# Performance work log

Measured on AMD Instinct MI355X. Metric: run time of the kernel, lower is better.

The kernel has to match this reference:

```python
import jax, jax.numpy as jnp
import numpy as np
import math

DIM = 1536
HEAD_DIM = 128
N_HEADS = DIM // HEAD_DIM
B, S = 2, 2048
F, H, W = 8, 16, 16  # F*H*W == S
MAX_POS = 1024
EPS = 1e-6


def _make_freqs():
    # complex rotary freqs per Wan convention, split [22,21,21] over head_dim/2=64
    c = HEAD_DIM // 2
    sizes = [c - 2 * (c // 3), c // 3, c // 3]
    theta = 10000.0
    parts = []
    for s in sizes:
        inv = 1.0 / theta ** (np.arange(s, dtype=np.float64) / s)
        ang = np.arange(MAX_POS, dtype=np.float64)[:, None] * inv[None, :]
        parts.append(np.stack([np.cos(ang), np.sin(ang)], axis=-1))
    return jnp.asarray(np.concatenate(parts, axis=1), dtype=jnp.float32)  # [MAX_POS, 64, 2]


def setup_inputs() -> dict:
    key = jax.random.key(0)
    ks = jax.random.split(key, 12)
    std = 1.0 / math.sqrt(DIM)
    inp = {
        "x": jax.random.normal(ks[0], (B, S, DIM), jnp.float32),
        "seq_lens": jnp.full((B,), S, jnp.int32),
        "grid_sizes": jnp.tile(jnp.array([[F, H, W]], jnp.int32), (B, 1)),
        "freqs": _make_freqs(),
        "Wq": jax.random.normal(ks[1], (DIM, DIM), jnp.float32) * std,
        "bq": jnp.zeros((DIM,), jnp.float32),
        "Wk": jax.random.normal(ks[2], (DIM, DIM), jnp.float32) * std,
        "bk": jnp.zeros((DIM,), jnp.float32),
        "Wv": jax.random.normal(ks[3], (DIM, DIM), jnp.float32) * std,
        "bv": jnp.zeros((DIM,), jnp.float32),
        "Wo": jax.random.normal(ks[4], (DIM, DIM), jnp.float32) * std,
        "bo": jnp.zeros((DIM,), jnp.float32),
        "wq_norm": jnp.ones((DIM,), jnp.float32),
        "wk_norm": jnp.ones((DIM,), jnp.float32),
    }
    return inp


def _rmsnorm(x, w):
    x32 = x.astype(jnp.float32)
    return x32 * jax.lax.rsqrt(jnp.mean(x32 * x32, axis=-1, keepdims=True) + EPS) * w


def _rope_apply(x, grid_sizes, freqs):
    # x: [B, S, N, D]; grid sizes uniform across batch -> vectorized (no per-sample loop)
    f, h, w = (int(v) for v in np.asarray(grid_sizes)[0])
    s_rot = f * h * w
    Bx, Sx, N, D = x.shape
    c = D // 2
    s0, s1 = c - 2 * (c // 3), c // 3
    cos, sin = freqs[..., 0], freqs[..., 1]

    def grid_cs(t):  # build [s_rot, c] table
        tf = jnp.broadcast_to(t[:f, None, None, :s0], (f, h, w, s0))
        th = jnp.broadcast_to(t[None, :h, None, s0:s0 + s1], (f, h, w, s1))
        tw = jnp.broadcast_to(t[None, None, :w, s0 + s1:s0 + 2 * s1], (f, h, w, s1))
        return jnp.concatenate([tf, th, tw], axis=-1).reshape(s_rot, 1, c)

    fc, fs = grid_cs(cos), grid_cs(sin)  # [s_rot, 1, c]
    xr = x[:, :s_rot].astype(jnp.float32).reshape(Bx, s_rot, N, c, 2)
    a, b = xr[..., 0], xr[..., 1]
    out = jnp.stack([a * fc - b * fs, a * fs + b * fc], axis=-1).reshape(Bx, s_rot, N, D)
    if s_rot < Sx:
        out = jnp.concatenate([out, x[:, s_rot:].astype(jnp.float32)], axis=1)
    return out


def reference(x, seq_lens, grid_sizes, freqs, Wq, bq, Wk, bk, Wv, bv, Wo, bo, wq_norm, wk_norm):
    Bx, Sx, dim = x.shape
    N, D = N_HEADS, HEAD_DIM
    q = _rmsnorm(x @ Wq.T + bq, wq_norm).reshape(Bx, Sx, N, D)
    k = _rmsnorm(x @ Wk.T + bk, wk_norm).reshape(Bx, Sx, N, D)
    v = (x @ Wv.T + bv).reshape(Bx, Sx, N, D)
    q = _rope_apply(q, grid_sizes, freqs)
    k = _rope_apply(k, grid_sizes, freqs)
    scores = jnp.einsum("bsnd,btnd->bnst", q, k) / math.sqrt(D)  # [B,N,S,S]
    kmask = jnp.arange(Sx)[None, :] < seq_lens[:, None]          # [B,S] over keys
    scores = jnp.where(kmask[:, None, None, :], scores, -1e30)
    attn = jax.nn.softmax(scores, axis=-1)
    out = jnp.einsum("bnst,btnd->bsnd", attn, v).reshape(Bx, Sx, dim)
    return out @ Wo.T + bo
```

## Files before the change

kernel.cpp:

```cpp
#include <hip/hip_runtime.h>

typedef __attribute__((ext_vector_type(8))) short bf16x8;
typedef __attribute__((ext_vector_type(8))) unsigned short ushort8;
typedef __attribute__((ext_vector_type(4))) float f32x4;
typedef __attribute__((ext_vector_type(16))) float f32x16;
typedef unsigned short u16;
typedef unsigned int u32;

__device__ inline float bf2f(u16 u) {
    unsigned int x = ((unsigned int)u) << 16;
    float f; __builtin_memcpy(&f, &x, 4); return f;
}
__device__ inline u16 f2bf(float f) {
    unsigned int x; __builtin_memcpy(&x, &f, 4);
    unsigned int r = (x + 0x7FFFu + ((x >> 16) & 1u)) >> 16;
    return (u16)r;
}
__device__ inline u32 cvtpk(float lo, float hi) {
    u32 r;
    asm("v_cvt_pk_bf16_f32 %0, %1, %2" : "=v"(r) : "v"(lo), "v"(hi));
    return r;
}
__device__ inline void store_out(u16* p, float v) { *p = f2bf(v); }
__device__ inline void store_out(float* p, float v) { *p = v; }

__global__ __launch_bounds__(256) void prep_kernel(const float* __restrict__ x,
                                                   const float* __restrict__ Wq, const float* __restrict__ Wk,
                                                   const float* __restrict__ Wv, const float* __restrict__ Wo,
                                                   const float* __restrict__ bq, const float* __restrict__ bk,
                                                   const float* __restrict__ bv, const float* __restrict__ freqs,
                                                   u16* __restrict__ xb,
                                                   u16* __restrict__ wqkv, u16* __restrict__ wob,
                                                   float* __restrict__ bqkv, float* __restrict__ rope) {
    int bid = blockIdx.x, t = threadIdx.x;
    if (bid < 7680) {
        const float* src;
        u16* dst;
        size_t j;
        if (bid < 3072) {
            src = x; dst = xb; j = (size_t)bid * 256 + t;
        } else {
            size_t i = (size_t)(bid - 3072) * 256 + t;
            int seg = (int)(i / 294912); j = i - (size_t)seg * 294912;
            src = (seg == 0) ? Wq : (seg == 1) ? Wk : (seg == 2) ? Wv : Wo;
            dst = (seg < 3) ? (wqkv + (size_t)seg * 2359296) : wob;
        }
        float4 a = *(const float4*)(src + j * 8);
        float4 b = *(const float4*)(src + j * 8 + 4);
        ushort8 o;
        o[0] = f2bf(a.x); o[1] = f2bf(a.y); o[2] = f2bf(a.z); o[3] = f2bf(a.w);
        o[4] = f2bf(b.x); o[5] = f2bf(b.y); o[6] = f2bf(b.z); o[7] = f2bf(b.w);
        *(ushort8*)(dst + j * 8) = o;
    } else if (bid < 8192) {
        int i = (bid - 7680) * 256 + t;
        int s = i >> 6, j = i & 63;
        int fi = s >> 8, hi = (s >> 4) & 15, wi = s & 15;
        int pos = (j < 22) ? fi : ((j < 43) ? hi : wi);
        rope[s * 128 + j * 2]     = freqs[pos * 128 + j * 2];
        rope[s * 128 + j * 2 + 1] = freqs[pos * 128 + j * 2 + 1];
    } else {
#pragma unroll
        for (int it = 0; it < 18; ++it) {
            int j = it * 256 + t;
            bqkv[j] = (j < 1536) ? bq[j] : ((j < 3072) ? bk[j - 1536] : bv[j - 3072]);
        }
    }
}

template <typename OutT>
__global__ __launch_bounds__(256) void gemm_db(const u16* __restrict__ A, const u16* __restrict__ Bw,
                                               const float* __restrict__ bias, OutT* __restrict__ C,
                                               int M, int N, int K) {
    __shared__ __align__(16) u16 As[2][4096];
    __shared__ __align__(16) u16 Bs[2][4096];
    const int tid = threadIdx.x;
    const int w = tid >> 6, l = tid & 63;
    const int lg = l >> 4, li = l & 15;
    const int row0 = blockIdx.x * 128, col0 = blockIdx.y * 128;
    const int wr = (w >> 1) * 64, wc = (w & 1) * 64;
    const int nt = K >> 5;

    f32x4 acc[4][4] = {};

    auto STAGE = [&](int bi, int t) {
        int k0 = t << 5;
#pragma unroll
        for (int c = 0; c < 2; ++c) {
            int idx = c * 256 + tid;
            int r = idx >> 2;
            int clog = (idx & 3) ^ ((r >> 1) & 3);
            __builtin_amdgcn_global_load_lds(
                (const __attribute__((address_space(1))) void*)(A + (size_t)(row0 + r) * K + k0 + clog * 8),
                (__attribute__((address_space(3))) void*)((char*)&As[0][0] + bi * 8192 + c * 4096 + w * 1024), 16, 0, 0);
            __builtin_amdgcn_global_load_lds(
                (const __attribute__((address_space(1))) void*)(Bw + (size_t)(col0 + r) * K + k0 + clog * 8),
                (__attribute__((address_space(3))) void*)((char*)&Bs[0][0] + bi * 8192 + c * 4096 + w * 1024), 16, 0, 0);
        }
    };

    const int rchunk = (lg ^ ((li >> 1) & 3)) * 8;
    STAGE(0, 0);
    for (int tb = 0; tb < nt; tb += 2) {
#pragma unroll
        for (int j = 0; j < 2; ++j) {
            const int t = tb + j;
            if (t + 1 < nt) {
                STAGE((j + 1) & 1, t + 1);
                asm volatile("s_waitcnt vmcnt(4)" ::: "memory");
            } else {
                asm volatile("s_waitcnt vmcnt(0)" ::: "memory");
            }
            __builtin_amdgcn_s_barrier();
            __builtin_amdgcn_sched_barrier(0);
            const u16* as = &As[j][0];
            const u16* bs = &Bs[j][0];
            bf16x8 af[4], bfr[4];
#pragma unroll
            for (int m = 0; m < 4; ++m) af[m] = *(const bf16x8*)(as + (wr + m * 16 + li) * 32 + rchunk);
#pragma unroll
            for (int n = 0; n < 4; ++n) bfr[n] = *(const bf16x8*)(bs + (wc + n * 16 + li) * 32 + rchunk);
#pragma unroll
            for (int m = 0; m < 4; ++m)
#pragma unroll
                for (int n = 0; n < 4; ++n)
                    acc[m][n] = __builtin_amdgcn_mfma_f32_16x16x32_bf16(af[m], bfr[n], acc[m][n], 0, 0, 0);
            __builtin_amdgcn_sched_barrier(0);
            __builtin_amdgcn_s_barrier();
        }
    }

#pragma unroll
    for (int m = 0; m < 4; ++m) {
#pragma unroll
        for (int n = 0; n < 4; ++n) {
#pragma unroll
            for (int j = 0; j < 4; ++j) {
                int r = row0 + wr + m * 16 + lg * 4 + j;
                int cc = col0 + wc + n * 16 + li;
                float v = acc[m][n][j] + bias[cc];
                store_out(&C[(size_t)r * N + cc], v);
            }
        }
    }
}

template <typename OutT>
__global__ __launch_bounds__(256) void gemm_bt(const u16* __restrict__ A, const u16* __restrict__ Bw,
                                               const float* __restrict__ bias, OutT* __restrict__ C,
                                               int M, int N, int K) {
    __shared__ __align__(16) u16 As[3][4096];
    __shared__ __align__(16) u16 Bs[3][4096];
    const int tid = threadIdx.x;
    const int w = tid >> 6, l = tid & 63;
    const int lg = l >> 4, li = l & 15;
    const int row0 = blockIdx.x * 128, col0 = blockIdx.y * 128;
    const int wr = (w >> 1) * 64, wc = (w & 1) * 64;
    const int nt = K >> 5;

    f32x4 acc[4][4] = {};

    auto STAGE = [&](int bi, int t) {
        int k0 = t << 5;
#pragma unroll
        for (int c = 0; c < 2; ++c) {
            int idx = c * 256 + tid;
            int r = idx >> 2;
            int clog = (idx & 3) ^ ((r >> 1) & 3);
            __builtin_amdgcn_global_load_lds(
                (const __attribute__((address_space(1))) void*)(A + (size_t)(row0 + r) * K + k0 + clog * 8),
                (__attribute__((address_space(3))) void*)((char*)&As[0][0] + bi * 8192 + c * 4096 + w * 1024), 16, 0, 0);
            __builtin_amdgcn_global_load_lds(
                (const __attribute__((address_space(1))) void*)(Bw + (size_t)(col0 + r) * K + k0 + clog * 8),
                (__attribute__((address_space(3))) void*)((char*)&Bs[0][0] + bi * 8192 + c * 4096 + w * 1024), 16, 0, 0);
        }
    };

    const int rchunk = (lg ^ ((li >> 1) & 3)) * 8;
    STAGE(0, 0);
    STAGE(1, 1);
    for (int tb = 0; tb < nt; tb += 3) {
#pragma unroll
        for (int j = 0; j < 3; ++j) {
            const int t = tb + j;
            if (t + 2 < nt) {
                STAGE((j + 2) % 3, t + 2);
                asm volatile("s_waitcnt vmcnt(8)" ::: "memory");
            } else if (t + 1 < nt) {
                asm volatile("s_waitcnt vmcnt(4)" ::: "memory");
            } else {
                asm volatile("s_waitcnt vmcnt(0)" ::: "memory");
            }
            __builtin_amdgcn_s_barrier();
            __builtin_amdgcn_sched_barrier(0);
            const u16* as = &As[j][0];
            const u16* bs = &Bs[j][0];
            bf16x8 af[4], bfr[4];
#pragma unroll
            for (int m = 0; m < 4; ++m) af[m] = *(const bf16x8*)(as + (wr + m * 16 + li) * 32 + rchunk);
#pragma unroll
            for (int n = 0; n < 4; ++n) bfr[n] = *(const bf16x8*)(bs + (wc + n * 16 + li) * 32 + rchunk);
#pragma unroll
            for (int m = 0; m < 4; ++m)
#pragma unroll
                for (int n = 0; n < 4; ++n)
                    acc[m][n] = __builtin_amdgcn_mfma_f32_16x16x32_bf16(af[m], bfr[n], acc[m][n], 0, 0, 0);
            __builtin_amdgcn_sched_barrier(0);
            __builtin_amdgcn_s_barrier();
        }
    }

#pragma unroll
    for (int m = 0; m < 4; ++m) {
#pragma unroll
        for (int n = 0; n < 4; ++n) {
#pragma unroll
            for (int j = 0; j < 4; ++j) {
                int r = row0 + wr + m * 16 + lg * 4 + j;
                int cc = col0 + wc + n * 16 + li;
                float v = acc[m][n][j] + bias[cc];
                store_out(&C[(size_t)r * N + cc], v);
            }
        }
    }
}

__global__ __launch_bounds__(256) void rmsview_kernel(const u16* __restrict__ qkv,
                                                      const float* __restrict__ wq_n,
                                                      const float* __restrict__ wk_n,
                                                      const float* __restrict__ rope,
                                                      u16* __restrict__ qh, u16* __restrict__ kh,
                                                      u16* __restrict__ vt) {
    __shared__ __align__(16) char sm[9216];
    int t = threadIdx.x;
    if (blockIdx.x < 4096) {
        int row = blockIdx.x;
        int b = row >> 11, s = row & 2047;
        const u16* pr = qkv + (size_t)row * 4608;
        int c0 = t * 6;

        float q[6], k[6];
#pragma unroll
        for (int i = 0; i < 3; ++i) {
            ushort2 uq = *(const ushort2*)(pr + c0 + 2 * i);
            ushort2 uk = *(const ushort2*)(pr + 1536 + c0 + 2 * i);
            q[2 * i] = bf2f(uq.x); q[2 * i + 1] = bf2f(uq.y);
            k[2 * i] = bf2f(uk.x); k[2 * i + 1] = bf2f(uk.y);
        }
        float sq = 0.f, sk = 0.f;
#pragma unroll
        for (int i = 0; i < 6; ++i) { sq += q[i] * q[i]; sk += k[i] * k[i]; }
#pragma unroll
        for (int off = 32; off >= 1; off >>= 1) {
            sq += __shfl_down(sq, off);
            sk += __shfl_down(sk, off);
        }
        float* red = (float*)sm;
        int w = t >> 6, l = t & 63;
        if (l == 0) { red[w] = sq; red[w + 4] = sk; }
        __syncthreads();
        float rq = rsqrtf((red[0] + red[1] + red[2] + red[3]) * (1.0f / 1536.0f) + 1e-6f);
        float rk = rsqrtf((red[4] + red[5] + red[6] + red[7]) * (1.0f / 1536.0f) + 1e-6f);

#pragma unroll
        for (int i = 0; i < 3; ++i) {
            int c = c0 + 2 * i;
            int h = c >> 7, d = c & 127;
            float cs = rope[s * 128 + d];
            float sn = rope[s * 128 + d + 1];
            float qa = q[2 * i] * rq * wq_n[c], qb = q[2 * i + 1] * rq * wq_n[c + 1];
            float ka = k[2 * i] * rk * wk_n[c], kb = k[2 * i + 1] * rk * wk_n[c + 1];
            size_t o = ((size_t)(b * 12 + h) * 2048 + s) * 128 + d;
            ushort2 qo, ko;
            qo.x = f2bf(qa * cs - qb * sn); qo.y = f2bf(qa * sn + qb * cs);
            ko.x = f2bf(ka * cs - kb * sn); ko.y = f2bf(ka * sn + kb * cs);
            *(ushort2*)(qh + o) = qo;
            *(ushort2*)(kh + o) = ko;
        }
    } else {
        int idx = blockIdx.x - 4096;
        const int s0 = (idx & 31) * 64;
        const int d0 = ((idx >> 5) & 1) * 64;
        const int bh = idx >> 6;
        const int b = bh / 12, h = bh % 12;
        u16* L = (u16*)sm;

#pragma unroll
        for (int j = 0; j < 2; ++j) {
            int p = j * 256 + t;
            int s = p >> 3, c8 = p & 7;
            ushort8 v8 = *(const ushort8*)(qkv + (size_t)(b * 2048 + s0 + s) * 4608 + 3072 + h * 128 + d0 + c8 * 8);
            int pb = c8 ^ ((s >> 3) & 7);
            *(ushort8*)(L + s * 72 + pb * 8) = v8;
        }
        __syncthreads();
#pragma unroll
        for (int j = 0; j < 2; ++j) {
            int p = j * 256 + t;
            int d = p >> 3, s8 = p & 7;
            ushort8 o;
#pragma unroll
            for (int i = 0; i < 8; ++i) {
                int ps = s8 * 8 + i;
                int v4 = ps & 15;
                int ls = (ps & ~15) | (v4 & 3) | ((v4 & 4) << 1) | ((v4 & 8) >> 1);
                o[i] = L[ls * 72 + ((((d >> 3) ^ (ls >> 3)) & 7) << 3) + (d & 7)];
            }
            *(ushort8*)(vt + (size_t)bh * 128 * 2048 + (size_t)(d0 + d) * 2048 + s0 + s8 * 8) = o;
        }
    }
}

__global__ __launch_bounds__(256, 2) void attn_kernel(const u16* __restrict__ qh, const u16* __restrict__ kh,
                                                      const u16* __restrict__ vt, const int* __restrict__ seq_lens,
                                                      u16* __restrict__ aout) {
    const int bid = blockIdx.x;
    const int g = bid & 7, rr = bid >> 3;
    const int bh = g * 3 + rr % 3;
    const int qt = rr / 3;
    const int b = bh / 12, h = bh % 12;
    const int tid = threadIdx.x;
    const int w = tid >> 6, l = tid & 63;
    const int q5 = l & 31;
    const int hi = l >> 5;
    const int seqlen = seq_lens[b];

    __shared__ __align__(16) char smem[65536];

    const size_t hbase = (size_t)bh * 2048 * 128;
    const u16* kb = kh + hbase;
    const u16* vtb = vt + hbase;

    const int qrow = qt * 128 + w * 32 + q5;
    bf16x8 qf[8];
    {
        const u16* qp = qh + hbase + (size_t)qrow * 128 + hi * 8;
#pragma unroll
        for (int kd = 0; kd < 8; ++kd) qf[kd] = *(const bf16x8*)(qp + kd * 16);
    }

    auto STAGE = [&](int bi, int kv0) {
#pragma unroll
        for (int i = 0; i < 4; ++i) {
            int p = i * 256 + tid;
            int kr = p >> 4, kc = p & 15;
            __builtin_amdgcn_global_load_lds(
                (const __attribute__((address_space(1))) void*)(kb + (size_t)(kv0 + kr) * 128 + ((kc ^ (kr & 15)) << 3)),
                (__attribute__((address_space(3))) void*)(smem + bi * 16384 + i * 4096 + w * 1024), 16, 0, 0);
            int vr = p >> 3, vc = p & 7;
            __builtin_amdgcn_global_load_lds(
                (const __attribute__((address_space(1))) void*)(vtb + (size_t)vr * 2048 + kv0 + ((vc ^ (vr & 7)) << 3)),
                (__attribute__((address_space(3))) void*)(smem + 32768 + bi * 16384 + i * 4096 + w * 1024), 16, 0, 0);
        }
    };

    f32x16 oacc[4] = {};
    float m_run = -3e38f, l_run = 0.f;
    const float c2 = 0.08838834764831845f * 1.44269504088896341f;

    STAGE(0, 0);
    for (int t = 0; t < 32; ++t) {
        const int cur = t & 1;
        const int kv0 = t * 64;
        if (t < 31) {
            STAGE(cur ^ 1, kv0 + 64);
            asm volatile("s_waitcnt vmcnt(8)" ::: "memory");
        } else {
            asm volatile("s_waitcnt vmcnt(0)" ::: "memory");
        }
        __builtin_amdgcn_s_barrier();
        __builtin_amdgcn_sched_barrier(0);

        const u16* Ks = (const u16*)(smem + cur * 16384);
        const u16* Vs = (const u16*)(smem + 32768 + cur * 16384);

        f32x16 sacc[2] = {};
        __builtin_amdgcn_s_setprio(1);
#pragma unroll
        for (int tt = 0; tt < 2; ++tt) {
            int row = tt * 32 + q5;
#pragma unroll
            for (int kd = 0; kd < 8; ++kd) {
                int bk = (2 * kd + hi) ^ (q5 & 15);
                bf16x8 kf = *(const bf16x8*)(Ks + row * 128 + bk * 8);
                sacc[tt] = __builtin_amdgcn_mfma_f32_32x32x16_bf16(kf, qf[kd], sacc[tt], 0, 0, 0);
            }
        }
        __builtin_amdgcn_s_setprio(0);

        if (kv0 + 64 > seqlen) {
#pragma unroll
            for (int tt = 0; tt < 2; ++tt)
#pragma unroll
                for (int m = 0; m < 4; ++m)
#pragma unroll
                    for (int r = 0; r < 4; ++r) {
                        int kv = kv0 + tt * 32 + m * 8 + hi * 4 + r;
                        if (kv >= seqlen) sacc[tt][m * 4 + r] = -1e30f;
                    }
        }

        float a8[8];
#pragma unroll
        for (int r = 0; r < 8; ++r)
            a8[r] = fmaxf(fmaxf(sacc[0][r], sacc[0][r + 8]), fmaxf(sacc[1][r], sacc[1][r + 8]));
        float b4_0 = fmaxf(a8[0], a8[1]), b4_1 = fmaxf(a8[2], a8[3]);
        float b4_2 = fmaxf(a8[4], a8[5]), b4_3 = fmaxf(a8[6], a8[7]);
        float pmax = fmaxf(fmaxf(b4_0, b4_1), fmaxf(b4_2, b4_3));
        pmax = fmaxf(pmax, __shfl_xor(pmax, 32));

        int defer = __all(pmax <= m_run + 62.7f);
        if (!defer) {
            float mnew = fmaxf(m_run, pmax);
            float alpha = __builtin_amdgcn_exp2f((m_run - mnew) * c2);
#pragma unroll
            for (int dt = 0; dt < 4; ++dt)
#pragma unroll
                for (int r = 0; r < 16; ++r) oacc[dt][r] *= alpha;
            l_run *= alpha;
            m_run = mnew;
        }

        float gs[8];
        u32 Wp[2][4][2];
#pragma unroll
        for (int tt = 0; tt < 2; ++tt)
#pragma unroll
            for (int m = 0; m < 4; ++m) {
                float p0 = __builtin_amdgcn_exp2f((sacc[tt][4 * m + 0] - m_run) * c2);
                float p1 = __builtin_amdgcn_exp2f((sacc[tt][4 * m + 1] - m_run) * c2);
                float p2 = __builtin_amdgcn_exp2f((sacc[tt][4 * m + 2] - m_run) * c2);
                float p3 = __builtin_amdgcn_exp2f((sacc[tt][4 * m + 3] - m_run) * c2);
                gs[tt * 4 + m] = (p0 + p1) + (p2 + p3);
                Wp[tt][m][0] = cvtpk(p0, p1);
                Wp[tt][m][1] = cvtpk(p2, p3);
            }
        float ls = ((gs[0] + gs[1]) + (gs[2] + gs[3])) + ((gs[4] + gs[5]) + (gs[6] + gs[7]));
        ls += __shfl_xor(ls, 32);
        l_run += ls;

        __builtin_amdgcn_s_setprio(1);
#pragma unroll
        for (int tt = 0; tt < 2; ++tt)
#pragma unroll
            for (int c = 0; c < 2; ++c) {
                union { u32 u[4]; bf16x8 v; } pu;
                pu.u[0] = Wp[tt][2 * c][0]; pu.u[1] = Wp[tt][2 * c][1];
                pu.u[2] = Wp[tt][2 * c + 1][0]; pu.u[3] = Wp[tt][2 * c + 1][1];
                int bk = 4 * tt + 2 * c + hi;
#pragma unroll
                for (int dt = 0; dt < 4; ++dt) {
                    int drow = dt * 32 + q5;
                    int pb = bk ^ (drow & 7);
                    bf16x8 vf = *(const bf16x8*)(Vs + drow * 64 + pb * 8);
                    oacc[dt] = __builtin_amdgcn_mfma_f32_32x32x16_bf16(vf, pu.v, oacc[dt], 0, 0, 0);
                }
            }
        __builtin_amdgcn_s_setprio(0);
        __builtin_amdgcn_sched_barrier(0);
        __builtin_amdgcn_s_barrier();
    }

    __syncthreads();
    u32* Lq = (u32*)smem + w * 2144;
    float inv_l = 1.0f / l_run;
#pragma unroll
    for (int dt = 0; dt < 4; ++dt)
#pragma unroll
        for (int m = 0; m < 4; ++m) {
            u32 w0 = cvtpk(oacc[dt][4 * m + 0] * inv_l, oacc[dt][4 * m + 1] * inv_l);
            u32 w1 = cvtpk(oacc[dt][4 * m + 2] * inv_l, oacc[dt][4 * m + 3] * inv_l);
            int widx = dt * 16 + 4 * m + 2 * hi;
            Lq[q5 * 67 + widx] = w0;
            Lq[q5 * 67 + widx + 1] = w1;
        }
    __builtin_amdgcn_s_waitcnt(0);
#pragma unroll
    for (int pp = 0; pp < 8; ++pp) {
        int qq = pp * 4 + (l >> 4);
        int cc = l & 15;
        union { u32 u[4]; ushort8 v; } ou;
        ou.u[0] = Lq[qq * 67 + cc * 4 + 0];
        ou.u[1] = Lq[qq * 67 + cc * 4 + 1];
        ou.u[2] = Lq[qq * 67 + cc * 4 + 2];
        ou.u[3] = Lq[qq * 67 + cc * 4 + 3];
        size_t off = ((size_t)(b * 2048 + qt * 128 + w * 32 + qq)) * 1536 + h * 128 + cc * 8;
        *(ushort8*)(aout + off) = ou.v;
    }
}

extern "C" void kernel_launch(void* const* d_in, const int* in_sizes, int n_in,
                              void* d_out, int out_size, void* d_ws, size_t ws_size,
                              hipStream_t stream) {
    const float* x    = (const float*)d_in[0];
    const int* seqlen = (const int*)d_in[1];
    const float* freqs = (const float*)d_in[3];
    const float* Wq = (const float*)d_in[4];  const float* bq = (const float*)d_in[5];
    const float* Wk = (const float*)d_in[6];  const float* bk = (const float*)d_in[7];
    const float* Wv = (const float*)d_in[8];  const float* bv = (const float*)d_in[9];
    const float* Wo = (const float*)d_in[10]; const float* bo = (const float*)d_in[11];
    const float* wqn = (const float*)d_in[12];
    const float* wkn = (const float*)d_in[13];
    float* out = (float*)d_out;

    char* ws = (char*)d_ws;
    u16*   xb   = (u16*)(ws);
    u16*   wqkv = (u16*)(ws + 12582912);
    u16*   wob  = (u16*)(ws + 26738688);
    float* bqkv = (float*)(ws + 31457280);
    float* rope = (float*)(ws + 31475712);
    u16*   qkv  = (u16*)(ws + 32524288);
    u16*   qhb  = (u16*)(ws + 70273024);
    u16*   khb  = (u16*)(ws + 82855936);
    u16*   vtb  = (u16*)(ws + 95438848);
    u16*   aob  = (u16*)(ws + 108021760);

    prep_kernel<<<8193, 256, 0, stream>>>(x, Wq, Wk, Wv, Wo, bq, bk, bv, freqs, xb, wqkv, wob, bqkv, rope);

    gemm_db<u16><<<dim3(32, 36), 256, 0, stream>>>(xb, wqkv, bqkv, qkv, 4096, 4608, 1536);
    rmsview_kernel<<<5632, 256, 0, stream>>>(qkv, wqn, wkn, rope, qhb, khb, vtb);
    attn_kernel<<<384, 256, 0, stream>>>(qhb, khb, vtb, seqlen, aob);
    gemm_bt<float><<<dim3(32, 12), 256, 0, stream>>>(aob, wob, bo, out, 4096, 1536, 1536);
}
```

Before: 215.5 us.

## Replace QKV GEMM with 256x256-tile, 8-wave phased pipelined kernel

The fused QKV projection GEMM moves from 128x128 tiles with 4 waves to 256x256 tiles with 8 waves and 128KB of LDS, staged as double-buffered 64-wide K slices split into four phases. Each phase interleaves the next tile's global-to-LDS loads with MFMA work on the current one, using s_setprio around the MFMA bursts. An XCD-aware block swizzle remaps block ids to output tiles. The larger tiles cut global and LDS traffic per FLOP, at the cost of only 288 blocks (little more than one wave on 256 CUs), lower occupancy from the big LDS footprint, and many barriers.

```diff
diff --git a/kernel.cpp b/kernel.cpp
--- a/kernel.cpp
+++ b/kernel.cpp
@@ -68,75 +68,130 @@
 }
 
 template <typename OutT>
-__global__ __launch_bounds__(256) void gemm_db(const u16* __restrict__ A, const u16* __restrict__ Bw,
-                                               const float* __restrict__ bias, OutT* __restrict__ C,
-                                               int M, int N, int K) {
-    __shared__ __align__(16) u16 As[2][4096];
-    __shared__ __align__(16) u16 Bs[2][4096];
+__global__ __launch_bounds__(512) void gemm256ph(const u16* __restrict__ A, const u16* __restrict__ Bw,
+                                                 const float* __restrict__ bias, OutT* __restrict__ C,
+                                                 int M, int N, int K, int nby) {
+    __shared__ __align__(16) char smem[131072];
     const int tid = threadIdx.x;
-    const int w = tid >> 6, l = tid & 63;
+    const int wid = tid >> 6, l = tid & 63;
+    const int wr = wid >> 2, wc = wid & 3;
     const int lg = l >> 4, li = l & 15;
-    const int row0 = blockIdx.x * 128, col0 = blockIdx.y * 128;
-    const int wr = (w >> 1) * 64, wc = (w & 1) * 64;
-    const int nt = K >> 5;
-
-    f32x4 acc[4][4] = {};
-
-    auto STAGE = [&](int bi, int t) {
-        int k0 = t << 5;
-#pragma unroll
-        for (int c = 0; c < 2; ++c) {
-            int idx = c * 256 + tid;
-            int r = idx >> 2;
-            int clog = (idx & 3) ^ ((r >> 1) & 3);
-            __builtin_amdgcn_global_load_lds(
-                (const __attribute__((address_space(1))) void*)(A + (size_t)(row0 + r) * K + k0 + clog * 8),
-                (__attribute__((address_space(3))) void*)((char*)&As[0][0] + bi * 8192 + c * 4096 + w * 1024), 16, 0, 0);
-            __builtin_amdgcn_global_load_lds(
-                (const __attribute__((address_space(1))) void*)(Bw + (size_t)(col0 + r) * K + k0 + clog * 8),
-                (__attribute__((address_space(3))) void*)((char*)&Bs[0][0] + bi * 8192 + c * 4096 + w * 1024), 16, 0, 0);
-        }
+    const int cpx = gridDim.x >> 3;
+    const int swz = ((int)blockIdx.x & 7) * cpx + ((int)blockIdx.x >> 3);
+    const int row0 = (swz / nby) * 256, col0 = (swz % nby) * 256;
+    const int NT = K >> 6;
+
+    f32x4 acc[8][4] = {};
+
+    auto STG = [&](int mat, int half, int kk, int t) {
+        const u16* src = mat ? Bw : A;
+        int r0g = (mat ? col0 : row0) + half * 128;
+        int row = tid >> 2;
+        int clog = (tid & 3) ^ ((row >> 1) & 3);
+        int base = (t & 1) * 65536 + mat * 32768 + half * 16384 + kk * 8192;
+        __builtin_amdgcn_global_load_lds(
+            (const __attribute__((address_space(1))) void*)(src + (size_t)(r0g + row) * K + t * 64 + kk * 32 + clog * 8),
+            (__attribute__((address_space(3))) void*)(smem + base + tid * 16), 16, 0, 0);
     };
-
     const int rchunk = (lg ^ ((li >> 1) & 3)) * 8;
-    STAGE(0, 0);
-    for (int tb = 0; tb < nt; tb += 2) {
-#pragma unroll
-        for (int j = 0; j < 2; ++j) {
-            const int t = tb + j;
-            if (t + 1 < nt) {
-                STAGE((j + 1) & 1, t + 1);
-                asm volatile("s_waitcnt vmcnt(4)" ::: "memory");
-            } else {
-                asm volatile("s_waitcnt vmcnt(0)" ::: "memory");
-            }
-            __builtin_amdgcn_s_barrier();
-            __builtin_amdgcn_sched_barrier(0);
-            const u16* as = &As[j][0];
-            const u16* bs = &Bs[j][0];
-            bf16x8 af[4], bfr[4];
-#pragma unroll
-            for (int m = 0; m < 4; ++m) af[m] = *(const bf16x8*)(as + (wr + m * 16 + li) * 32 + rchunk);
-#pragma unroll
-            for (int n = 0; n < 4; ++n) bfr[n] = *(const bf16x8*)(bs + (wc + n * 16 + li) * 32 + rchunk);
-#pragma unroll
-            for (int m = 0; m < 4; ++m)
-#pragma unroll
-                for (int n = 0; n < 4; ++n)
-                    acc[m][n] = __builtin_amdgcn_mfma_f32_16x16x32_bf16(af[m], bfr[n], acc[m][n], 0, 0, 0);
-            __builtin_amdgcn_sched_barrier(0);
-            __builtin_amdgcn_s_barrier();
-        }
-    }
-
-#pragma unroll
-    for (int m = 0; m < 4; ++m) {
+    auto LDA = [&](bf16x8* af, int t, int kk, int mh) {
+        const u16* R = (const u16*)(smem + (t & 1) * 65536 + wr * 16384 + kk * 8192);
+#pragma unroll
+        for (int mm = 0; mm < 4; ++mm) {
+            int row = (mh * 4 + mm) * 16 + li;
+            af[mm] = *(const bf16x8*)(R + row * 32 + rchunk);
+        }
+    };
+    auto LDB = [&](bf16x8* bf, int t, int kk) {
+        const u16* R = (const u16*)(smem + (t & 1) * 65536 + 32768 + (wc >> 1) * 16384 + kk * 8192);
+#pragma unroll
+        for (int nn = 0; nn < 4; ++nn) {
+            int row = (wc & 1) * 64 + nn * 16 + li;
+            bf[nn] = *(const bf16x8*)(R + row * 32 + rchunk);
+        }
+    };
+
+    STG(0, 0, 0, 0); STG(0, 1, 0, 0);
+    STG(1, 0, 0, 0); STG(1, 1, 0, 0);
+    STG(0, 0, 1, 0); STG(0, 1, 1, 0);
+    STG(1, 0, 1, 0); STG(1, 1, 1, 0);
+    asm volatile("s_waitcnt vmcnt(4)" ::: "memory");
+    __builtin_amdgcn_s_barrier();
+    __builtin_amdgcn_sched_barrier(0);
+
+    bf16x8 af[4], bf[4];
+    for (int t = 0; t < NT; ++t) {
+        const int more = (t + 1 < NT);
+        LDA(af, t, 0, 0); LDB(bf, t, 0);
+        if (more) { STG(0, 0, 0, t + 1); STG(0, 1, 0, t + 1); }
+        __builtin_amdgcn_s_barrier();
+        asm volatile("s_waitcnt lgkmcnt(0)" ::: "memory");
+        __builtin_amdgcn_sched_barrier(0);
+        __builtin_amdgcn_s_setprio(1);
+#pragma unroll
+        for (int mm = 0; mm < 4; ++mm)
+#pragma unroll
+            for (int nn = 0; nn < 4; ++nn)
+                acc[mm][nn] = __builtin_amdgcn_mfma_f32_16x16x32_bf16(af[mm], bf[nn], acc[mm][nn], 0, 0, 0);
+        __builtin_amdgcn_s_setprio(0);
+        __builtin_amdgcn_sched_barrier(0);
+        __builtin_amdgcn_s_barrier();
+        LDA(af, t, 0, 1);
+        if (more) { STG(1, 0, 0, t + 1); STG(1, 1, 0, t + 1);
+                    asm volatile("s_waitcnt vmcnt(4)" ::: "memory"); }
+        else      { asm volatile("s_waitcnt vmcnt(0)" ::: "memory"); }
+        __builtin_amdgcn_s_barrier();
+        asm volatile("s_waitcnt lgkmcnt(0)" ::: "memory");
+        __builtin_amdgcn_sched_barrier(0);
+        __builtin_amdgcn_s_setprio(1);
+#pragma unroll
+        for (int mm = 0; mm < 4; ++mm)
+#pragma unroll
+            for (int nn = 0; nn < 4; ++nn)
+                acc[4 + mm][nn] = __builtin_amdgcn_mfma_f32_16x16x32_bf16(af[mm], bf[nn], acc[4 + mm][nn], 0, 0, 0);
+        __builtin_amdgcn_s_setprio(0);
+        __builtin_amdgcn_sched_barrier(0);
+        __builtin_amdgcn_s_barrier();
+        LDA(af, t, 1, 0); LDB(bf, t, 1);
+        if (more) { STG(0, 0, 1, t + 1); STG(0, 1, 1, t + 1); }
+        __builtin_amdgcn_s_barrier();
+        asm volatile("s_waitcnt lgkmcnt(0)" ::: "memory");
+        __builtin_amdgcn_sched_barrier(0);
+        __builtin_amdgcn_s_setprio(1);
+#pragma unroll
+        for (int mm = 0; mm < 4; ++mm)
+#pragma unroll
+            for (int nn = 0; nn < 4; ++nn)
+                acc[mm][nn] = __builtin_amdgcn_mfma_f32_16x16x32_bf16(af[mm], bf[nn], acc[mm][nn], 0, 0, 0);
+        __builtin_amdgcn_s_setprio(0);
+        __builtin_amdgcn_sched_barrier(0);
+        __builtin_amdgcn_s_barrier();
+        LDA(af, t, 1, 1);
+        if (more) { STG(1, 0, 1, t + 1); STG(1, 1, 1, t + 1);
+                    asm volatile("s_waitcnt vmcnt(4)" ::: "memory"); }
+        else      { asm volatile("s_waitcnt vmcnt(0)" ::: "memory"); }
+        __builtin_amdgcn_s_barrier();
+        asm volatile("s_waitcnt lgkmcnt(0)" ::: "memory");
+        __builtin_amdgcn_sched_barrier(0);
+        __builtin_amdgcn_s_setprio(1);
+#pragma unroll
+        for (int mm = 0; mm < 4; ++mm)
+#pragma unroll
+            for (int nn = 0; nn < 4; ++nn)
+                acc[4 + mm][nn] = __builtin_amdgcn_mfma_f32_16x16x32_bf16(af[mm], bf[nn], acc[4 + mm][nn], 0, 0, 0);
+        __builtin_amdgcn_s_setprio(0);
+        __builtin_amdgcn_sched_barrier(0);
+        __builtin_amdgcn_s_barrier();
+    }
+
+#pragma unroll
+    for (int m = 0; m < 8; ++m) {
 #pragma unroll
         for (int n = 0; n < 4; ++n) {
 #pragma unroll
             for (int j = 0; j < 4; ++j) {
-                int r = row0 + wr + m * 16 + lg * 4 + j;
-                int cc = col0 + wc + n * 16 + li;
+                int r = row0 + wr * 128 + m * 16 + lg * 4 + j;
+                int cc = col0 + wc * 64 + n * 16 + li;
                 float v = acc[m][n][j] + bias[cc];
                 store_out(&C[(size_t)r * N + cc], v);
             }
@@ -516,7 +571,7 @@
 
     prep_kernel<<<8193, 256, 0, stream>>>(x, Wq, Wk, Wv, Wo, bq, bk, bv, freqs, xb, wqkv, wob, bqkv, rope);
 
-    gemm_db<u16><<<dim3(32, 36), 256, 0, stream>>>(xb, wqkv, bqkv, qkv, 4096, 4608, 1536);
+    gemm256ph<u16><<<288, 512, 0, stream>>>(xb, wqkv, bqkv, qkv, 4096, 4608, 1536, 18);
     rmsview_kernel<<<5632, 256, 0, stream>>>(qkv, wqn, wkn, rope, qhb, khb, vtb);
     attn_kernel<<<384, 256, 0, stream>>>(qhb, khb, vtb, seqlen, aob);
     gemm_bt<float><<<dim3(32, 12), 256, 0, stream>>>(aob, wob, bo, out, 4096, 1536, 1536);
```

After: 230.1 us. 6.8% more time.
